# Kernel optimization log

Hardware: AMD Instinct MI355X
Metric: run time of the kernel (lower is better)

Reference implementation:

```python
import jax, jax.numpy as jnp
import numpy as np

UNITS = 64
CHANNEL = 64
L1 = 32
L2 = 32
BATCH = 64


def setup_inputs() -> dict:
    key = jax.random.key(0)
    k1, k2, k3, k4, k5 = jax.random.split(key, 5)
    input_dim = CHANNEL + 3 * UNITS
    inputs = jax.random.normal(k1, (BATCH, CHANNEL, L1, L2), dtype=jnp.float32)
    W = jax.random.normal(k2, (input_dim, UNITS * 7), dtype=jnp.float32) * (1.0 / np.sqrt(input_dim))
    U_rec = jax.random.normal(k3, (UNITS * 3, UNITS), dtype=jnp.float32) * (1.0 / np.sqrt(UNITS * 3))
    bias = jnp.zeros((UNITS * 8,), dtype=jnp.float32)
    W_ij = jax.random.normal(k4, (CHANNEL, UNITS), dtype=jnp.float32) * (1.0 / np.sqrt(CHANNEL))
    return {"inputs": inputs, "W": W, "U_rec": U_rec, "bias": bias, "W_ij": W_ij}


def reference(inputs, W, U_rec, bias, W_ij):
    B, C, l1, l2 = inputs.shape
    u = W_ij.shape[1]
    wr, br = W[:, : 3 * u], bias[: 3 * u]
    wz, bz = W[:, 3 * u : 7 * u], bias[3 * u : 7 * u]
    b_ij = bias[7 * u :]

    # [L1*L2, B, C] scan order: row-major over (i, j), direction 'lt'
    x = jnp.transpose(inputs, (2, 3, 0, 1)).reshape(l1 * l2, B, C)
    states0 = jnp.zeros((l1 + 1, l2 + 1, B, u), dtype=inputs.dtype)  # zero boundary

    def step(carry, xs):
        states, _ = carry
        s_ij, t = xs
        i = t // l2
        j = t % l2
        h_diag = states[i, j]        # [B, u]
        h_top = states[i, j + 1]
        h_left = states[i + 1, j]
        # q = [h_top, h_left, h_diag, s_ij] : [B, 3u + C]
        q = jnp.concatenate([h_top, h_left, h_diag, s_ij], axis=1)
        r = jax.nn.sigmoid(q @ wr + br)                     # [B, 3u]
        z = q @ wz + bz                                     # [B, 4u]
        zg = jax.nn.softmax(z.reshape(B, 4, u), axis=1)     # softmax across 4 gates per unit
        zi, zl, zt, zd = zg[:, 0], zg[:, 1], zg[:, 2], zg[:, 3]
        h_hat = jnp.tanh(
            s_ij @ W_ij + b_ij
            + (r * jnp.concatenate([h_left, h_top, h_diag], axis=1)) @ U_rec
        )
        h_ij = zl * h_left + zt * h_top + zd * h_diag + zi * h_hat
        states = states.at[i + 1, j + 1].set(h_ij)
        return (states, h_ij), None

    tsteps = jnp.arange(l1 * l2)
    (_, h_last), _ = jax.lax.scan(
        step, (states0, jnp.zeros((B, u), dtype=inputs.dtype)), (x, tsteps)
    )
    return h_last
```

## Files before the change

### kernel.cpp

```cpp
#include <hip/hip_runtime.h>
#include <cstdint>
#include <cstddef>


#define LDIM   32
#define BATCH  64
#define UNITS  64
#define CHAN   64
#define NBT    4
#define BT     16
#define TPB    512

typedef _Float16 f16;
typedef _Float16 f16x8 __attribute__((ext_vector_type(8)));
typedef float    f32x4 __attribute__((ext_vector_type(4)));

__global__ __launch_bounds__(TPB, 2) void spatial_gru_kernel(
    const float* __restrict__ x,
    const float* __restrict__ W,
    const float* __restrict__ Urec,
    const float* __restrict__ bias,
    const float* __restrict__ Wij,
    float* __restrict__ out,
    uint32_t* __restrict__ hbuf)
{
    const int bid = blockIdx.x;
    const int row = bid >> 2;
    const int bt  = bid & 3;
    const int b0  = bt * BT;
    const int t   = (int)threadIdx.x;
    const int u   = t & 63;
    const int g   = t >> 6;
    const int l15 = t & 15;
    const int lq  = (t & 63) >> 4;

    __shared__ __attribute__((aligned(16))) f16 qf[BT][264];
    __shared__ __attribute__((aligned(16))) f16 rf[BT][200];
    __shared__ float qs32[BT][204];
    __shared__ float Gsz [BT][260];
    __shared__ float pacc[4][BT][68];

    f16x8 wreg[4][8];
    float bias1[4] = {0.f, 0.f, 0.f, 0.f};
    if (g < 7) {
        const int nb = g * 64 + l15;
#pragma unroll
        for (int T = 0; T < 4; ++T) {
            bias1[T] = bias[nb + 16 * T];
#pragma unroll
            for (int s = 0; s < 8; ++s) {
                f16x8 v;
#pragma unroll
                for (int jj = 0; jj < 8; ++jj) {
                    int kk = s * 32 + lq * 8 + jj;
                    v[jj] = (f16)W[(size_t)kk * 448 + nb + 16 * T];
                }
                wreg[T][s] = v;
            }
        }
    }
    f16x8 wreg2[4][2];
    {
        const int kb = (g & 3) * 64;
#pragma unroll
        for (int T = 0; T < 4; ++T) {
            const int nn = T * 16 + l15;
#pragma unroll
            for (int s = 0; s < 2; ++s) {
                f16x8 v;
#pragma unroll
                for (int jj = 0; jj < 8; ++jj) {
                    int kk = kb + s * 32 + lq * 8 + jj;
                    float wv = (kk < 192) ? Urec[kk * 64 + nn] : Wij[(kk - 192) * 64 + nn];
                    v[jj] = (f16)wv;
                }
                wreg2[T][s] = v;
            }
        }
    }
    const float bij = bias[448 + u];

    for (int idx = t; idx < 192 * BT; idx += TPB) {
        int b = idx & 15, k = idx >> 4;
        qs32[b][k] = 0.f;
        qf[b][k] = (f16)0.f;
    }

    const size_t xb0 = (size_t)(b0 + g) * 65536 + (size_t)u * 1024 + (size_t)row * 32;
    const size_t xb1 = xb0 + (size_t)8 * 65536;
    {
        float x0 = x[xb0], x1 = x[xb1];
        qf[g][192 + u]     = (f16)x0;
        qf[g + 8][192 + u] = (f16)x1;
    }
    __syncthreads();

    for (int j = 0; j < LDIM; ++j) {
        float ht0 = 0.f, ht1 = 0.f;
        f16 hf0 = (f16)0.f, hf1 = (f16)0.f;
        if (row > 0) {
            const uint32_t* sp =
                hbuf + ((((size_t)(row - 1) * LDIM + j) * NBT + bt) << 9) + (g << 6) + u;
            uint32_t w = __hip_atomic_load(sp, __ATOMIC_RELAXED, __HIP_MEMORY_SCOPE_AGENT);
            while ((w & 0x00010001u) != 0x00010001u) {
                __builtin_amdgcn_s_sleep(1);
                w = __hip_atomic_load(sp, __ATOMIC_RELAXED, __HIP_MEMORY_SCOPE_AGENT);
            }
            uint16_t lo = (uint16_t)(w & 0xFFFFu), hi = (uint16_t)(w >> 16);
            hf0 = __builtin_bit_cast(f16, lo);
            hf1 = __builtin_bit_cast(f16, hi);
            ht0 = (float)hf0;
            ht1 = (float)hf1;
        }
        qs32[g][u]     = ht0;  qf[g][u]     = hf0;
        qs32[g + 8][u] = ht1;  qf[g + 8][u] = hf1;
        __syncthreads();

        float nx0 = 0.f, nx1 = 0.f;
        if (j < LDIM - 1) { nx0 = x[xb0 + j + 1]; nx1 = x[xb1 + j + 1]; }

        if (g < 7) {
            f32x4 acc[4];
#pragma unroll
            for (int T = 0; T < 4; ++T)
                acc[T] = (f32x4){bias1[T], bias1[T], bias1[T], bias1[T]};
#pragma unroll
            for (int s = 0; s < 8; ++s) {
                f16x8 a = *(const f16x8*)&qf[l15][s * 32 + lq * 8];
#pragma unroll
                for (int T = 0; T < 4; ++T)
                    acc[T] = __builtin_amdgcn_mfma_f32_16x16x32_f16(a, wreg[T][s], acc[T], 0, 0, 0);
            }
            if (g < 3) {
                const int colbase = (g == 0) ? 64 : (g == 1) ? 0 : 128;
#pragma unroll
                for (int T = 0; T < 4; ++T)
#pragma unroll
                    for (int r = 0; r < 4; ++r) {
                        float rr = 1.f / (1.f + __expf(-acc[T][r]));
                        int b = lq * 4 + r;
                        float hv = qs32[b][colbase + T * 16 + l15];
                        rf[b][g * 64 + T * 16 + l15] = (f16)(rr * hv);
                    }
            } else {
                const int zb = (g - 3) * 64;
#pragma unroll
                for (int T = 0; T < 4; ++T)
#pragma unroll
                    for (int r = 0; r < 4; ++r)
                        Gsz[lq * 4 + r][zb + T * 16 + l15] = acc[T][r];
            }
        } else {
            f32x4 a2[4];
#pragma unroll
            for (int T = 0; T < 4; ++T) a2[T] = (f32x4){0.f, 0.f, 0.f, 0.f};
#pragma unroll
            for (int s = 0; s < 2; ++s) {
                f16x8 a = *(const f16x8*)&qf[l15][192 + s * 32 + lq * 8];
#pragma unroll
                for (int T = 0; T < 4; ++T)
                    a2[T] = __builtin_amdgcn_mfma_f32_16x16x32_f16(a, wreg2[T][s], a2[T], 0, 0, 0);
            }
#pragma unroll
            for (int T = 0; T < 4; ++T)
#pragma unroll
                for (int r = 0; r < 4; ++r)
                    pacc[3][lq * 4 + r][T * 16 + l15] = a2[T][r];
        }
        __syncthreads();

        if (g >= 4 && g < 7) {
            const int w  = g - 4;
            const int kb = w * 64;
            f32x4 a2[4];
#pragma unroll
            for (int T = 0; T < 4; ++T) a2[T] = (f32x4){0.f, 0.f, 0.f, 0.f};
#pragma unroll
            for (int s = 0; s < 2; ++s) {
                f16x8 a = *(const f16x8*)&rf[l15][kb + s * 32 + lq * 8];
#pragma unroll
                for (int T = 0; T < 4; ++T)
                    a2[T] = __builtin_amdgcn_mfma_f32_16x16x32_f16(a, wreg2[T][s], a2[T], 0, 0, 0);
            }
#pragma unroll
            for (int T = 0; T < 4; ++T)
#pragma unroll
                for (int r = 0; r < 4; ++r)
                    pacc[w][lq * 4 + r][T * 16 + l15] = a2[T][r];
        }
        __syncthreads();

        float hvv[2], hTv[2];
#pragma unroll
        for (int i = 0; i < 2; ++i) {
            int b = g + 8 * i;
            float hhv = bij + pacc[0][b][u] + pacc[1][b][u] + pacc[2][b][u] + pacc[3][b][u];
            float e2 = __expf(2.f * hhv);
            float th = 1.f - 2.f / (e2 + 1.f);
            float zi = Gsz[b][u],       zl = Gsz[b][64 + u];
            float zt = Gsz[b][128 + u], zd = Gsz[b][192 + u];
            float mx = fmaxf(fmaxf(zi, zl), fmaxf(zt, zd));
            float ei = __expf(zi - mx), el = __expf(zl - mx);
            float et = __expf(zt - mx), ed = __expf(zd - mx);
            float inv = 1.f / (ei + el + et + ed);
            float hT = qs32[b][u], hL = qs32[b][64 + u], hD = qs32[b][128 + u];
            float hv = (el * hL + et * hT + ed * hD + ei * th) * inv;
            hvv[i] = hv; hTv[i] = hT;
        }
        {
            uint16_t lo = (uint16_t)(__builtin_bit_cast(uint16_t, (f16)hvv[0]) | 1u);
            uint16_t hi = (uint16_t)(__builtin_bit_cast(uint16_t, (f16)hvv[1]) | 1u);
            uint32_t pw = ((uint32_t)hi << 16) | lo;
            __hip_atomic_store(
                hbuf + ((((size_t)row * LDIM + j) * NBT + bt) << 9) + (g << 6) + u,
                pw, __ATOMIC_RELAXED, __HIP_MEMORY_SCOPE_AGENT);
        }
        if (row == LDIM - 1 && j == LDIM - 1) {
            out[(size_t)(b0 + g) * UNITS + u]     = hvv[0];
            out[(size_t)(b0 + g + 8) * UNITS + u] = hvv[1];
        }
#pragma unroll
        for (int i = 0; i < 2; ++i) {
            int b = g + 8 * i;
            qs32[b][128 + u] = hTv[i];
            qs32[b][64 + u]  = hvv[i];
            f16 htf = qf[b][u];
            qf[b][128 + u] = htf;
            qf[b][64 + u]  = (f16)hvv[i];
        }
        qf[g][192 + u]     = (f16)nx0;
        qf[g + 8][192 + u] = (f16)nx1;
    }
}

extern "C" void kernel_launch(void* const* d_in, const int* in_sizes, int n_in,
                              void* d_out, int out_size, void* d_ws, size_t ws_size,
                              hipStream_t stream) {
    const float* x    = (const float*)d_in[0];
    const float* W    = (const float*)d_in[1];
    const float* Urec = (const float*)d_in[2];
    const float* bias = (const float*)d_in[3];
    const float* Wij  = (const float*)d_in[4];
    float* out = (float*)d_out;

    uint32_t* hbuf = (uint32_t*)d_ws;

    spatial_gru_kernel<<<LDIM * NBT, TPB, 0, stream>>>(
        x, W, Urec, bias, Wij, out, hbuf);
}
```

Before: 263.7 us.

## Restructure per-step schedule: precompute next-step gate partials, rotate state buffers, merge h_hat GEMM

Splits the gate GEMM so the contributions that only depend on h_left and the next x are computed ahead for the following column, leaving only the h_top/h_diag part on the critical path. Warp 7 now computes the whole h_hat pre-activation (including bias and the Wij term) in one pass, replacing the partial-sum buffer and one synchronisation. State buffers are ring-rotated by index instead of copied each step, and the wait on the upstream row is moved to the end of the iteration so it happens before the barrier. The cost is a more complex indexing scheme and extra shared-memory footprint.

```diff
diff --git a/kernel.cpp b/kernel.cpp
--- a/kernel.cpp
+++ b/kernel.cpp
@@ -4,9 +4,6 @@
 
 
 #define LDIM   32
-#define BATCH  64
-#define UNITS  64
-#define CHAN   64
 #define NBT    4
 #define BT     16
 #define TPB    512
@@ -14,6 +11,9 @@
 typedef _Float16 f16;
 typedef _Float16 f16x8 __attribute__((ext_vector_type(8)));
 typedef float    f32x4 __attribute__((ext_vector_type(4)));
+
+#define LD_AGENT(p)   __hip_atomic_load((p), __ATOMIC_RELAXED, __HIP_MEMORY_SCOPE_AGENT)
+#define ST_AGENT(p,v) __hip_atomic_store((p), (v), __ATOMIC_RELAXED, __HIP_MEMORY_SCOPE_AGENT)
 
 __global__ __launch_bounds__(TPB, 2) void spatial_gru_kernel(
     const float* __restrict__ x,
@@ -25,23 +25,18 @@
     uint32_t* __restrict__ hbuf)
 {
     const int bid = blockIdx.x;
-    const int row = bid >> 2;
-    const int bt  = bid & 3;
-    const int b0  = bt * BT;
-    const int t   = (int)threadIdx.x;
-    const int u   = t & 63;
-    const int g   = t >> 6;
-    const int l15 = t & 15;
-    const int lq  = (t & 63) >> 4;
-
-    __shared__ __attribute__((aligned(16))) f16 qf[BT][264];
+    const int row = bid >> 2, bt = bid & 3, b0 = bt * BT;
+    const int t = (int)threadIdx.x, u = t & 63, g = t >> 6;
+    const int l15 = t & 15, lq = (t & 63) >> 4;
+
+    __shared__ __attribute__((aligned(16))) f16 qf[BT][328];
     __shared__ __attribute__((aligned(16))) f16 rf[BT][200];
-    __shared__ float qs32[BT][204];
+    __shared__ float qs32[BT][260];
     __shared__ float Gsz [BT][260];
-    __shared__ float pacc[4][BT][68];
+    __shared__ float hh  [BT][68];
 
     f16x8 wreg[4][8];
-    float bias1[4] = {0.f, 0.f, 0.f, 0.f};
+    float bias1[4];
     if (g < 7) {
         const int nb = g * 64 + l15;
 #pragma unroll
@@ -58,89 +53,97 @@
                 wreg[T][s] = v;
             }
         }
-    }
-    f16x8 wreg2[4][2];
-    {
-        const int kb = (g & 3) * 64;
+    } else {
 #pragma unroll
         for (int T = 0; T < 4; ++T) {
             const int nn = T * 16 + l15;
-#pragma unroll
-            for (int s = 0; s < 2; ++s) {
+            bias1[T] = bias[448 + nn];
+#pragma unroll
+            for (int s = 0; s < 8; ++s) {
                 f16x8 v;
 #pragma unroll
                 for (int jj = 0; jj < 8; ++jj) {
-                    int kk = kb + s * 32 + lq * 8 + jj;
+                    int kk = s * 32 + lq * 8 + jj;
                     float wv = (kk < 192) ? Urec[kk * 64 + nn] : Wij[(kk - 192) * 64 + nn];
                     v[jj] = (f16)wv;
                 }
-                wreg2[T][s] = v;
-            }
-        }
-    }
-    const float bij = bias[448 + u];
-
-    for (int idx = t; idx < 192 * BT; idx += TPB) {
+                wreg[T][s] = v;
+            }
+        }
+    }
+
+    for (int idx = t; idx < 256 * BT; idx += TPB) {
         int b = idx & 15, k = idx >> 4;
         qs32[b][k] = 0.f;
-        qf[b][k] = (f16)0.f;
-    }
-
-    const size_t xb0 = (size_t)(b0 + g) * 65536 + (size_t)u * 1024 + (size_t)row * 32;
-    const size_t xb1 = xb0 + (size_t)8 * 65536;
-    {
-        float x0 = x[xb0], x1 = x[xb1];
-        qf[g][192 + u]     = (f16)x0;
-        qf[g + 8][192 + u] = (f16)x1;
+        if (k < 192) qf[b][k] = (f16)0.f;
+    }
+
+    const float* xg0 = x + (size_t)(b0 + g) * 65536 + (size_t)u * 1024 + (size_t)row * 32;
+    const float* xg1 = xg0 + (size_t)8 * 65536;
+    qf[g][192 + u]     = (f16)xg0[0];  qf[g + 8][192 + u] = (f16)xg1[0];
+    qf[g][256 + u]     = (f16)xg0[1];  qf[g + 8][256 + u] = (f16)xg1[1];
+    float xv0 = xg0[2], xv1 = xg1[2];
+    if (row > 0) {
+        const uint32_t* sp = hbuf + (((size_t)((row - 1) * LDIM) * NBT + bt) << 9) + (g << 6) + u;
+        uint32_t w = LD_AGENT(sp);
+        while ((w & 0x00010001u) != 0x00010001u) {
+            __builtin_amdgcn_s_sleep(1);
+            w = LD_AGENT(sp);
+        }
+        f16 h0 = __builtin_bit_cast(f16, (uint16_t)(w & 0xFFFFu));
+        f16 h1 = __builtin_bit_cast(f16, (uint16_t)(w >> 16));
+        qf[g][u] = h0;            qf[g + 8][u] = h1;
+        qs32[g][u] = (float)h0;   qs32[g + 8][u] = (float)h1;
     }
     __syncthreads();
 
+    f32x4 acc[4];
+    if (g < 7) {
+#pragma unroll
+        for (int T = 0; T < 4; ++T)
+            acc[T] = (f32x4){bias1[T], bias1[T], bias1[T], bias1[T]};
+#pragma unroll
+        for (int sv = 0; sv < 2; ++sv) {
+            f16x8 a4 = *(const f16x8*)&qf[l15][64 + sv * 32 + lq * 8];
+            f16x8 a6 = *(const f16x8*)&qf[l15][192 + sv * 32 + lq * 8];
+#pragma unroll
+            for (int T = 0; T < 4; ++T) {
+                acc[T] = __builtin_amdgcn_mfma_f32_16x16x32_f16(a4, wreg[T][4 + sv], acc[T], 0, 0, 0);
+                acc[T] = __builtin_amdgcn_mfma_f32_16x16x32_f16(a6, wreg[T][6 + sv], acc[T], 0, 0, 0);
+            }
+        }
+    }
+
     for (int j = 0; j < LDIM; ++j) {
-        float ht0 = 0.f, ht1 = 0.f;
-        f16 hf0 = (f16)0.f, hf1 = (f16)0.f;
-        if (row > 0) {
-            const uint32_t* sp =
-                hbuf + ((((size_t)(row - 1) * LDIM + j) * NBT + bt) << 9) + (g << 6) + u;
-            uint32_t w = __hip_atomic_load(sp, __ATOMIC_RELAXED, __HIP_MEMORY_SCOPE_AGENT);
-            while ((w & 0x00010001u) != 0x00010001u) {
-                __builtin_amdgcn_s_sleep(1);
-                w = __hip_atomic_load(sp, __ATOMIC_RELAXED, __HIP_MEMORY_SCOPE_AGENT);
-            }
-            uint16_t lo = (uint16_t)(w & 0xFFFFu), hi = (uint16_t)(w >> 16);
-            hf0 = __builtin_bit_cast(f16, lo);
-            hf1 = __builtin_bit_cast(f16, hi);
-            ht0 = (float)hf0;
-            ht1 = (float)hf1;
-        }
-        qs32[g][u]     = ht0;  qf[g][u]     = hf0;
-        qs32[g + 8][u] = ht1;  qf[g + 8][u] = hf1;
-        __syncthreads();
-
-        float nx0 = 0.f, nx1 = 0.f;
-        if (j < LDIM - 1) { nx0 = x[xb0 + j + 1]; nx1 = x[xb1 + j + 1]; }
+        const int par  = j & 1;
+        const int hTq  = par << 6;
+        const int hTqn = (1 - par) << 6;
+        const int sq   = 192 + (par << 6);
+        const int sqn  = 192 + ((1 - par) << 6);
+        const int s3   = (j % 3) * 64;
+        const int s3p  = ((j + 2) % 3) * 64;
+        const int s3n  = ((j + 1) % 3) * 64;
 
         if (g < 7) {
-            f32x4 acc[4];
-#pragma unroll
-            for (int T = 0; T < 4; ++T)
-                acc[T] = (f32x4){bias1[T], bias1[T], bias1[T], bias1[T]};
-#pragma unroll
-            for (int s = 0; s < 8; ++s) {
-                f16x8 a = *(const f16x8*)&qf[l15][s * 32 + lq * 8];
-#pragma unroll
-                for (int T = 0; T < 4; ++T)
-                    acc[T] = __builtin_amdgcn_mfma_f32_16x16x32_f16(a, wreg[T][s], acc[T], 0, 0, 0);
+#pragma unroll
+            for (int sv = 0; sv < 2; ++sv) {
+                f16x8 a0 = *(const f16x8*)&qf[l15][hTq + sv * 32 + lq * 8];
+                f16x8 a2 = *(const f16x8*)&qf[l15][128 + sv * 32 + lq * 8];
+#pragma unroll
+                for (int T = 0; T < 4; ++T) {
+                    acc[T] = __builtin_amdgcn_mfma_f32_16x16x32_f16(a0, wreg[T][0 + sv], acc[T], 0, 0, 0);
+                    acc[T] = __builtin_amdgcn_mfma_f32_16x16x32_f16(a2, wreg[T][2 + sv], acc[T], 0, 0, 0);
+                }
             }
             if (g < 3) {
-                const int colbase = (g == 0) ? 64 : (g == 1) ? 0 : 128;
+                const int colbase = (g == 0) ? 192 : (g == 1) ? s3 : s3p;
 #pragma unroll
                 for (int T = 0; T < 4; ++T)
 #pragma unroll
                     for (int r = 0; r < 4; ++r) {
                         float rr = 1.f / (1.f + __expf(-acc[T][r]));
                         int b = lq * 4 + r;
-                        float hv = qs32[b][colbase + T * 16 + l15];
-                        rf[b][g * 64 + T * 16 + l15] = (f16)(rr * hv);
+                        rf[b][g * 64 + T * 16 + l15] = (f16)(rr * qs32[b][colbase + T * 16 + l15]);
                     }
             } else {
                 const int zb = (g - 3) * 64;
@@ -151,51 +154,57 @@
                         Gsz[lq * 4 + r][zb + T * 16 + l15] = acc[T][r];
             }
         } else {
-            f32x4 a2[4];
-#pragma unroll
-            for (int T = 0; T < 4; ++T) a2[T] = (f32x4){0.f, 0.f, 0.f, 0.f};
-#pragma unroll
-            for (int s = 0; s < 2; ++s) {
-                f16x8 a = *(const f16x8*)&qf[l15][192 + s * 32 + lq * 8];
-#pragma unroll
-                for (int T = 0; T < 4; ++T)
-                    a2[T] = __builtin_amdgcn_mfma_f32_16x16x32_f16(a, wreg2[T][s], a2[T], 0, 0, 0);
-            }
 #pragma unroll
             for (int T = 0; T < 4; ++T)
+                acc[T] = (f32x4){bias1[T], bias1[T], bias1[T], bias1[T]};
+#pragma unroll
+            for (int sv = 0; sv < 2; ++sv) {
+                f16x8 a = *(const f16x8*)&qf[l15][sq + sv * 32 + lq * 8];
+#pragma unroll
+                for (int T = 0; T < 4; ++T)
+                    acc[T] = __builtin_amdgcn_mfma_f32_16x16x32_f16(a, wreg[T][6 + sv], acc[T], 0, 0, 0);
+            }
+        }
+        __syncthreads();
+
+        if (g < 7) {
+            if (j < LDIM - 1) {
+#pragma unroll
+                for (int T = 0; T < 4; ++T)
+                    acc[T] = (f32x4){bias1[T], bias1[T], bias1[T], bias1[T]};
+#pragma unroll
+                for (int sv = 0; sv < 2; ++sv) {
+                    f16x8 a4 = *(const f16x8*)&qf[l15][hTq + sv * 32 + lq * 8];
+                    f16x8 a6 = *(const f16x8*)&qf[l15][sqn + sv * 32 + lq * 8];
+#pragma unroll
+                    for (int T = 0; T < 4; ++T) {
+                        acc[T] = __builtin_amdgcn_mfma_f32_16x16x32_f16(a4, wreg[T][4 + sv], acc[T], 0, 0, 0);
+                        acc[T] = __builtin_amdgcn_mfma_f32_16x16x32_f16(a6, wreg[T][6 + sv], acc[T], 0, 0, 0);
+                    }
+                }
+            }
+        } else {
+#pragma unroll
+            for (int s = 0; s < 6; ++s) {
+                f16x8 a = *(const f16x8*)&rf[l15][s * 32 + lq * 8];
+#pragma unroll
+                for (int T = 0; T < 4; ++T)
+                    acc[T] = __builtin_amdgcn_mfma_f32_16x16x32_f16(a, wreg[T][s], acc[T], 0, 0, 0);
+            }
+#pragma unroll
+            for (int T = 0; T < 4; ++T)
 #pragma unroll
                 for (int r = 0; r < 4; ++r)
-                    pacc[3][lq * 4 + r][T * 16 + l15] = a2[T][r];
+                    hh[lq * 4 + r][T * 16 + l15] = acc[T][r];
         }
         __syncthreads();
 
-        if (g >= 4 && g < 7) {
-            const int w  = g - 4;
-            const int kb = w * 64;
-            f32x4 a2[4];
-#pragma unroll
-            for (int T = 0; T < 4; ++T) a2[T] = (f32x4){0.f, 0.f, 0.f, 0.f};
-#pragma unroll
-            for (int s = 0; s < 2; ++s) {
-                f16x8 a = *(const f16x8*)&rf[l15][kb + s * 32 + lq * 8];
-#pragma unroll
-                for (int T = 0; T < 4; ++T)
-                    a2[T] = __builtin_amdgcn_mfma_f32_16x16x32_f16(a, wreg2[T][s], a2[T], 0, 0, 0);
-            }
-#pragma unroll
-            for (int T = 0; T < 4; ++T)
-#pragma unroll
-                for (int r = 0; r < 4; ++r)
-                    pacc[w][lq * 4 + r][T * 16 + l15] = a2[T][r];
-        }
-        __syncthreads();
-
-        float hvv[2], hTv[2];
+        float hvv[2];
 #pragma unroll
         for (int i = 0; i < 2; ++i) {
-            int b = g + 8 * i;
-            float hhv = bij + pacc[0][b][u] + pacc[1][b][u] + pacc[2][b][u] + pacc[3][b][u];
-            float e2 = __expf(2.f * hhv);
+            const int b = g + 8 * i;
+            float hl = hh[b][u];
+            float e2 = __expf(2.f * hl);
             float th = 1.f - 2.f / (e2 + 1.f);
             float zi = Gsz[b][u],       zl = Gsz[b][64 + u];
             float zt = Gsz[b][128 + u], zd = Gsz[b][192 + u];
@@ -203,33 +212,41 @@
             float ei = __expf(zi - mx), el = __expf(zl - mx);
             float et = __expf(zt - mx), ed = __expf(zd - mx);
             float inv = 1.f / (ei + el + et + ed);
-            float hT = qs32[b][u], hL = qs32[b][64 + u], hD = qs32[b][128 + u];
+            float hT = qs32[b][s3 + u], hL = qs32[b][192 + u], hD = qs32[b][s3p + u];
             float hv = (el * hL + et * hT + ed * hD + ei * th) * inv;
-            hvv[i] = hv; hTv[i] = hT;
-        }
-        {
-            uint16_t lo = (uint16_t)(__builtin_bit_cast(uint16_t, (f16)hvv[0]) | 1u);
-            uint16_t hi = (uint16_t)(__builtin_bit_cast(uint16_t, (f16)hvv[1]) | 1u);
-            uint32_t pw = ((uint32_t)hi << 16) | lo;
-            __hip_atomic_store(
-                hbuf + ((((size_t)row * LDIM + j) * NBT + bt) << 9) + (g << 6) + u,
-                pw, __ATOMIC_RELAXED, __HIP_MEMORY_SCOPE_AGENT);
+            hvv[i] = hv;
+            qs32[b][192 + u] = hv;
+            qf[b][128 + u]   = (f16)hv;
+        }
+        if (row < LDIM - 1) {
+            uint32_t lo = (uint32_t)(__builtin_bit_cast(uint16_t, (f16)hvv[0]) | 1u);
+            uint32_t hi = (uint32_t)(__builtin_bit_cast(uint16_t, (f16)hvv[1]) | 1u);
+            ST_AGENT(hbuf + (((size_t)(row * LDIM + j) * NBT + bt) << 9) + (g << 6) + u,
+                     (hi << 16) | lo);
         }
         if (row == LDIM - 1 && j == LDIM - 1) {
-            out[(size_t)(b0 + g) * UNITS + u]     = hvv[0];
-            out[(size_t)(b0 + g + 8) * UNITS + u] = hvv[1];
-        }
-#pragma unroll
-        for (int i = 0; i < 2; ++i) {
-            int b = g + 8 * i;
-            qs32[b][128 + u] = hTv[i];
-            qs32[b][64 + u]  = hvv[i];
-            f16 htf = qf[b][u];
-            qf[b][128 + u] = htf;
-            qf[b][64 + u]  = (f16)hvv[i];
-        }
-        qf[g][192 + u]     = (f16)nx0;
-        qf[g + 8][192 + u] = (f16)nx1;
+            out[(size_t)(b0 + g) * 64 + u]     = hvv[0];
+            out[(size_t)(b0 + g + 8) * 64 + u] = hvv[1];
+        }
+        if (j < LDIM - 2) {
+            qf[g][sq + u]     = (f16)xv0;
+            qf[g + 8][sq + u] = (f16)xv1;
+            if (j < LDIM - 3) { xv0 = xg0[j + 3]; xv1 = xg1[j + 3]; }
+        }
+        if (row > 0 && j < LDIM - 1) {
+            const uint32_t* sp =
+                hbuf + (((size_t)((row - 1) * LDIM + j + 1) * NBT + bt) << 9) + (g << 6) + u;
+            uint32_t w = LD_AGENT(sp);
+            while ((w & 0x00010001u) != 0x00010001u) {
+                __builtin_amdgcn_s_sleep(1);
+                w = LD_AGENT(sp);
+            }
+            f16 h0 = __builtin_bit_cast(f16, (uint16_t)(w & 0xFFFFu));
+            f16 h1 = __builtin_bit_cast(f16, (uint16_t)(w >> 16));
+            qf[g][hTqn + u] = h0;          qf[g + 8][hTqn + u] = h1;
+            qs32[g][s3n + u] = (float)h0;  qs32[g + 8][s3n + u] = (float)h1;
+        }
+        __syncthreads();
     }
 }
 
```

After: 270.7 us. +2.6%, slower.
